# Optimization experiments

Hardware: AMD Instinct MI355X
Metric: run time of the kernel (lower is better)

Reference implementation:

```python
import jax, jax.numpy as jnp
import numpy as np

NUM_HEADS = 8
CHUNK = 64
TOP_K = 5


def setup_inputs() -> dict:
    key = jax.random.key(0)
    ks = jax.random.split(key, 5)
    D = 512
    x = jax.random.normal(ks[0], (1, 2048, D), dtype=jnp.float32)
    s = 0.02
    Wq = jax.random.normal(ks[1], (D, D), dtype=jnp.float32) * s
    Wk = jax.random.normal(ks[2], (D, D), dtype=jnp.float32) * s
    Wv = jax.random.normal(ks[3], (D, D), dtype=jnp.float32) * s
    Wo = jax.random.normal(ks[4], (D, D), dtype=jnp.float32) * s
    return {"x": x, "Wq": Wq, "Wk": Wk, "Wv": Wv, "Wo": Wo}


def reference(x, Wq, Wk, Wv, Wo):
    B, S, D = x.shape
    H = NUM_HEADS
    hd = D // H
    scale = hd ** -0.5
    C = S // CHUNK  # number of chunks

    def split_heads(t):
        return t.reshape(B, S, H, hd).transpose(0, 2, 1, 3)  # [B,H,S,hd]

    Q = split_heads(x @ Wq)
    K = split_heads(x @ Wk)
    V = split_heads(x @ Wv)

    # chunked K/V: [B,H,C,chunk,hd]
    Kc = K.reshape(B, H, C, CHUNK, hd)
    Vc = V.reshape(B, H, C, CHUNK, hd)

    # chunk descriptors: mean-pooled keys per chunk -> [B,H,C,hd]
    chunk_keys = Kc.mean(axis=3)

    # route each query to top-k chunks by scaled similarity
    sims = jnp.einsum('bhsd,bhcd->bhsc', Q, chunk_keys) * scale  # [B,H,S,C]
    _, idx = jax.lax.top_k(sims, TOP_K)  # [B,H,S,K]

    # gather selected K/V chunk blocks: [B,H,S,K,chunk,hd]
    idx_flat = idx.reshape(B, H, S * TOP_K)[:, :, :, None, None]
    Kg = jnp.take_along_axis(Kc, idx_flat, axis=2).reshape(B, H, S, TOP_K, CHUNK, hd)
    Vg = jnp.take_along_axis(Vc, idx_flat, axis=2).reshape(B, H, S, TOP_K, CHUNK, hd)

    # sparse block attention over the K*chunk gathered keys per query
    scores = jnp.einsum('bhsd,bhskcd->bhskc', Q, Kg) * scale
    attn = jax.nn.softmax(scores.reshape(B, H, S, TOP_K * CHUNK), axis=-1)
    attn = attn.reshape(B, H, S, TOP_K, CHUNK)
    out = jnp.einsum('bhskc,bhskcd->bhsd', attn, Vg)  # [B,H,S,hd]

    out = out.transpose(0, 2, 1, 3).reshape(B, S, D)
    return out @ Wo
```

## Files before the change

kernel.cpp:

```cpp
#include <hip/hip_runtime.h>
#include <hip/hip_bf16.h>
#include <math.h>

#define S_LEN 2048
#define D_DIM 512
#define H_NUM 8
#define HD    64
#define C_NUM 32
#define TOPK  5
#define SCALE 0.125f
#define QCAP  1024
#define ATILES 16

typedef __attribute__((ext_vector_type(8))) short bf16x8;
typedef __attribute__((ext_vector_type(4))) float f32x4;

__device__ __forceinline__ unsigned short f2b(float f) {
    __hip_bfloat16 h = __float2bfloat16(f);
    unsigned short u;
    __builtin_memcpy(&u, &h, 2);
    return u;
}
__device__ __forceinline__ bf16x8 pack8(float4 a, float4 b) {
    bf16x8 r;
    r[0] = (short)f2b(a.x); r[1] = (short)f2b(a.y);
    r[2] = (short)f2b(a.z); r[3] = (short)f2b(a.w);
    r[4] = (short)f2b(b.x); r[5] = (short)f2b(b.y);
    r[6] = (short)f2b(b.z); r[7] = (short)f2b(b.w);
    return r;
}
__device__ __forceinline__ float b2f(unsigned short u) {
    __hip_bfloat16 h;
    __builtin_memcpy(&h, &u, 2);
    return __bfloat162float(h);
}

#define BM 64
#define BN 64
#define BK 32

__device__ __forceinline__ void gemm_body(const float* __restrict__ A,
                                          const float* __restrict__ B,
                                          float* __restrict__ C,
                                          int M, int N, int K,
                                          int bx, int by) {
    __shared__ float As[BK][BM + 4];
    __shared__ float Bs[BK][BN];

    const int t  = threadIdx.x;
    const int tx = t & 15;
    const int ty = t >> 4;
    const int m0 = by * BM;
    const int n0 = bx * BN;

    float4 acc0 = make_float4(0.f,0.f,0.f,0.f);
    float4 acc1 = make_float4(0.f,0.f,0.f,0.f);
    float4 acc2 = make_float4(0.f,0.f,0.f,0.f);
    float4 acc3 = make_float4(0.f,0.f,0.f,0.f);

    const int ar = t >> 3;
    const int ac = (t & 7) * 4;
    const int br = t >> 4;
    const int bc = (t & 15) * 4;

    float4 a0, a1, b0, b1;
    auto LD = [&](int k0) {
        a0 = *(const float4*)&A[(size_t)(m0 + ar)      * K + k0 + ac];
        a1 = *(const float4*)&A[(size_t)(m0 + ar + 32) * K + k0 + ac];
        b0 = *(const float4*)&B[(size_t)(k0 + br)      * N + n0 + bc];
        b1 = *(const float4*)&B[(size_t)(k0 + br + 16) * N + n0 + bc];
    };

    LD(0);
    for (int k0 = 0; k0 < K; k0 += BK) {
        __syncthreads();
        As[ac+0][ar]    = a0.x; As[ac+1][ar]    = a0.y; As[ac+2][ar]    = a0.z; As[ac+3][ar]    = a0.w;
        As[ac+0][ar+32] = a1.x; As[ac+1][ar+32] = a1.y; As[ac+2][ar+32] = a1.z; As[ac+3][ar+32] = a1.w;
        *(float4*)&Bs[br][bc]      = b0;
        *(float4*)&Bs[br + 16][bc] = b1;
        __syncthreads();

        if (k0 + BK < K) LD(k0 + BK);

        #pragma unroll
        for (int kk = 0; kk < BK; ++kk) {
            float4 a = *(const float4*)&As[kk][ty * 4];
            float4 b = *(const float4*)&Bs[kk][tx * 4];
            acc0.x += a.x*b.x; acc0.y += a.x*b.y; acc0.z += a.x*b.z; acc0.w += a.x*b.w;
            acc1.x += a.y*b.x; acc1.y += a.y*b.y; acc1.z += a.y*b.z; acc1.w += a.y*b.w;
            acc2.x += a.z*b.x; acc2.y += a.z*b.y; acc2.z += a.z*b.z; acc2.w += a.z*b.w;
            acc3.x += a.w*b.x; acc3.y += a.w*b.y; acc3.z += a.w*b.z; acc3.w += a.w*b.w;
        }
    }

    *(float4*)&C[(size_t)(m0 + ty*4 + 0) * N + n0 + tx*4] = acc0;
    *(float4*)&C[(size_t)(m0 + ty*4 + 1) * N + n0 + tx*4] = acc1;
    *(float4*)&C[(size_t)(m0 + ty*4 + 2) * N + n0 + tx*4] = acc2;
    *(float4*)&C[(size_t)(m0 + ty*4 + 3) * N + n0 + tx*4] = acc3;
}

__device__ __forceinline__ void gemm_v_body(const float* __restrict__ A,
                                            const float* __restrict__ B,
                                            unsigned short* __restrict__ C,
                                            int M, int N, int K,
                                            int bx, int by) {
    __shared__ unsigned short Asv[64][72];
    __shared__ unsigned short Bsv[64][72];

    const int t  = threadIdx.x;
    const int m0 = by * 64;
    const int n0 = bx * 64;
    const int rl = t >> 2;
    const int c4 = (t & 3) * 16;

    const int lane = t & 63, w = t >> 6, lr = lane & 15, quad = lane >> 4;

    f32x4 acc[4] = {{0.f,0.f,0.f,0.f},{0.f,0.f,0.f,0.f},
                    {0.f,0.f,0.f,0.f},{0.f,0.f,0.f,0.f}};

    float4 fa[4], fb[4];
    auto LDA = [&](int k0) {
        const float* p = &A[(size_t)(m0 + rl) * K + k0 + c4];
        fa[0] = *(const float4*)&p[0];  fa[1] = *(const float4*)&p[4];
        fa[2] = *(const float4*)&p[8];  fa[3] = *(const float4*)&p[12];
    };
    auto LDB = [&](int k0) {
        const float* p = &B[(size_t)(k0 + rl) * N + n0 + c4];
        fb[0] = *(const float4*)&p[0];  fb[1] = *(const float4*)&p[4];
        fb[2] = *(const float4*)&p[8];  fb[3] = *(const float4*)&p[12];
    };

    LDA(0); LDB(0);
    for (int k0 = 0; k0 < K; k0 += 64) {
        __syncthreads();
        *(bf16x8*)&Asv[rl][c4]     = pack8(fa[0], fa[1]);
        *(bf16x8*)&Asv[rl][c4 + 8] = pack8(fa[2], fa[3]);
        #pragma unroll
        for (int f = 0; f < 4; ++f) {
            float4 v = fb[f];
            Bsv[c4 + f*4 + 0][rl] = f2b(v.x);
            Bsv[c4 + f*4 + 1][rl] = f2b(v.y);
            Bsv[c4 + f*4 + 2][rl] = f2b(v.z);
            Bsv[c4 + f*4 + 3][rl] = f2b(v.w);
        }
        __syncthreads();

        if (k0 + 64 < K) { LDA(k0 + 64); LDB(k0 + 64); }

        bf16x8 a0 = *(const bf16x8*)&Asv[w * 16 + lr][quad * 8];
        bf16x8 a1 = *(const bf16x8*)&Asv[w * 16 + lr][32 + quad * 8];
        #pragma unroll
        for (int nt = 0; nt < 4; ++nt) {
            bf16x8 b0 = *(const bf16x8*)&Bsv[nt * 16 + lr][quad * 8];
            bf16x8 b1 = *(const bf16x8*)&Bsv[nt * 16 + lr][32 + quad * 8];
            acc[nt] = __builtin_amdgcn_mfma_f32_16x16x32_bf16(a0, b0, acc[nt], 0, 0, 0);
            acc[nt] = __builtin_amdgcn_mfma_f32_16x16x32_bf16(a1, b1, acc[nt], 0, 0, 0);
        }
    }

    #pragma unroll
    for (int nt = 0; nt < 4; ++nt)
        #pragma unroll
        for (int r = 0; r < 4; ++r) {
            int m = m0 + w * 16 + quad * 4 + r;
            int n = n0 + nt * 16 + lr;
            C[(size_t)m * N + n] = f2b(acc[nt][r]);
        }
}

__global__ __launch_bounds__(256) void gemm_qkvz(const float* __restrict__ x,
                                                 const float* __restrict__ Wq,
                                                 const float* __restrict__ Wk,
                                                 const float* __restrict__ Wv,
                                                 float* __restrict__ Qb,
                                                 float* __restrict__ Kb,
                                                 unsigned short* __restrict__ Vbf,
                                                 int* __restrict__ cur) {
    if (blockIdx.z == 2) {
        if (blockIdx.x == 0 && blockIdx.y == 0) cur[threadIdx.x] = 0;
        gemm_v_body(x, Wv, Vbf, S_LEN, D_DIM, D_DIM, blockIdx.x, blockIdx.y);
    } else {
        const float* B = (blockIdx.z == 0) ? Wq : Wk;
        float*       C = (blockIdx.z == 0) ? Qb : Kb;
        gemm_body(x, B, C, S_LEN, D_DIM, D_DIM, blockIdx.x, blockIdx.y);
    }
}

__global__ __launch_bounds__(256) void chunk_keys_kernel(const float* __restrict__ K,
                                                         float* __restrict__ ck) {
    int i = blockIdx.x * 256 + threadIdx.x;
    int c = i >> 9;
    int d = i & 511;
    const float* p = K + (size_t)c * 64 * D_DIM + d;
    float sum = 0.f;
    #pragma unroll
    for (int r = 0; r < 64; ++r) sum += p[(size_t)r * D_DIM];
    ck[(size_t)c * D_DIM + d] = sum * (1.0f / 64.0f);
}

__global__ __launch_bounds__(256) void sims_topk(const float* __restrict__ Q,
                                                 const float* __restrict__ ck,
                                                 int* __restrict__ cur,
                                                 unsigned short* __restrict__ qlist) {
    __shared__ float qtile[64][68];
    __shared__ float cks[32][68];
    __shared__ float simsb[64][36];
    __shared__ int   lds_cnt[32];
    __shared__ int   lds_base[32];

    const int t  = threadIdx.x;
    const int s0 = blockIdx.x * 64;
    const int h  = blockIdx.y;

    if (t < 32) lds_cnt[t] = 0;

    {
        int r = t >> 2;
        #pragma unroll
        for (int i = 0; i < 4; ++i) {
            int cf4 = (t & 3) * 4 + i;
            *(float4*)&qtile[r][cf4 * 4] =
                *(const float4*)&Q[(size_t)(s0 + r) * D_DIM + h * HD + cf4 * 4];
        }
    }
    for (int i = t; i < C_NUM * 16; i += 256) {
        int c = i >> 4, df4 = i & 15;
        *(float4*)&cks[c][df4 * 4] =
            *(const float4*)&ck[(size_t)c * D_DIM + h * HD + df4 * 4];
    }
    __syncthreads();

    {
        const int sl = t >> 2, g = t & 3;
        float sa[8] = {0.f,0.f,0.f,0.f,0.f,0.f,0.f,0.f};
        #pragma unroll
        for (int d4 = 0; d4 < 16; ++d4) {
            float4 q4 = *(const float4*)&qtile[sl][d4 * 4];
            #pragma unroll
            for (int j = 0; j < 8; ++j) {
                float4 c4 = *(const float4*)&cks[g * 8 + j][d4 * 4];
                sa[j] += q4.x*c4.x + q4.y*c4.y + q4.z*c4.z + q4.w*c4.w;
            }
        }
        *(float4*)&simsb[sl][g*8 + 0] = make_float4(sa[0], sa[1], sa[2], sa[3]);
        *(float4*)&simsb[sl][g*8 + 4] = make_float4(sa[4], sa[5], sa[6], sa[7]);
    }
    __syncthreads();

    int csel[TOPK], lpos[TOPK];
    if (t < 64) {
        float sv[32];
        #pragma unroll
        for (int cq = 0; cq < 8; ++cq) {
            float4 v = *(const float4*)&simsb[t][cq * 4];
            sv[cq*4+0] = v.x; sv[cq*4+1] = v.y; sv[cq*4+2] = v.z; sv[cq*4+3] = v.w;
        }
        #pragma unroll
        for (int k = 0; k < TOPK; ++k) {
            float best = -INFINITY; int bi = 0;
            #pragma unroll
            for (int cc = 0; cc < 32; ++cc) {
                bool gt = sv[cc] > best;
                best = gt ? sv[cc] : best;
                bi   = gt ? cc : bi;
            }
            #pragma unroll
            for (int cc = 0; cc < 32; ++cc)
                if (cc == bi) sv[cc] = -INFINITY;
            csel[k] = bi;
            lpos[k] = atomicAdd(&lds_cnt[bi], 1);
        }
    }
    __syncthreads();

    if (t < 32) lds_base[t] = atomicAdd(&cur[h * 32 + t], lds_cnt[t]);
    __syncthreads();

    if (t < 64) {
        #pragma unroll
        for (int k = 0; k < TOPK; ++k) {
            int c = csel[k];
            int pos = lds_base[c] + lpos[k];
            if (pos < QCAP)
                qlist[(size_t)(h * 32 + c) * QCAP + pos] =
                    (unsigned short)((s0 + t) | (k << 11));
        }
    }
}

__global__ __launch_bounds__(256) void moc_attn6(const float* __restrict__ Q,
                                                 const float* __restrict__ K,
                                                 const unsigned short* __restrict__ Vbf,
                                                 const int* __restrict__ cnt,
                                                 const unsigned short* __restrict__ qlist,
                                                 float* __restrict__ lpart,
                                                 float* __restrict__ Opart) {
    __shared__ unsigned short Qs[64][72];
    __shared__ unsigned short Ks[64][72];
    __shared__ unsigned short VT[64][72];
    __shared__ unsigned short Ps[64][72];
    __shared__ unsigned short slist[64];

    const int hc = blockIdx.y;
    const int h  = hc >> 5;
    const int c  = hc & 31;
    const int g  = blockIdx.x;
    const int t  = threadIdx.x;

    const int count = min(cnt[hc], QCAP);
    const int base  = g * 64;
    if (base >= count) return;
    const int lim = min(count - base, 64);

    const float* Kb = K + ((size_t)c * 64) * D_DIM + h * HD;
    const unsigned short* Vb = Vbf + ((size_t)c * 64) * D_DIM + h * HD;
    const unsigned short* list = qlist + (size_t)hc * QCAP + base;

    {
        const int j  = t >> 2;
        const int d0 = (t & 3) * 16;

        const float* kr = Kb + (size_t)j * D_DIM + d0;
        float4 k0 = *(const float4*)&kr[0],  k1 = *(const float4*)&kr[4];
        float4 k2 = *(const float4*)&kr[8],  k3 = *(const float4*)&kr[12];
        *(bf16x8*)&Ks[j][d0]     = pack8(k0, k1);
        *(bf16x8*)&Ks[j][d0 + 8] = pack8(k2, k3);

        const unsigned short* vr = Vb + (size_t)j * D_DIM + d0;
        bf16x8 v0 = *(const bf16x8*)&vr[0];
        bf16x8 v1 = *(const bf16x8*)&vr[8];
        #pragma unroll
        for (int i = 0; i < 8; ++i) {
            VT[d0 + i][j]     = (unsigned short)v0[i];
            VT[d0 + 8 + i][j] = (unsigned short)v1[i];
        }

        unsigned short pv = (j < lim) ? list[j] : (unsigned short)0xFFFF;
        if ((t & 3) == 0) slist[j] = pv;
        int s = (pv == 0xFFFF) ? 0 : (int)(pv & 2047);
        const float* qr = Q + (size_t)s * D_DIM + h * HD + d0;
        float4 q0 = *(const float4*)&qr[0],  q1 = *(const float4*)&qr[4];
        float4 q2 = *(const float4*)&qr[8],  q3 = *(const float4*)&qr[12];
        *(bf16x8*)&Qs[j][d0]     = pack8(q0, q1);
        *(bf16x8*)&Qs[j][d0 + 8] = pack8(q2, q3);
    }
    __syncthreads();

    const int lane = t & 63;
    const int w    = t >> 6;
    const int lr   = lane & 15;
    const int quad = lane >> 4;

    bf16x8 aq0 = *(const bf16x8*)&Qs[w * 16 + lr][quad * 8];
    bf16x8 aq1 = *(const bf16x8*)&Qs[w * 16 + lr][32 + quad * 8];

    f32x4 acc[4];
    #pragma unroll
    for (int kt = 0; kt < 4; ++kt) {
        bf16x8 b0 = *(const bf16x8*)&Ks[kt * 16 + lr][quad * 8];
        bf16x8 b1 = *(const bf16x8*)&Ks[kt * 16 + lr][32 + quad * 8];
        f32x4 z = {0.f, 0.f, 0.f, 0.f};
        z = __builtin_amdgcn_mfma_f32_16x16x32_bf16(aq0, b0, z, 0, 0, 0);
        z = __builtin_amdgcn_mfma_f32_16x16x32_bf16(aq1, b1, z, 0, 0, 0);
        acc[kt] = z;
    }

    unsigned short pb[4][4];
    float dsum[4] = {0.f, 0.f, 0.f, 0.f};
    #pragma unroll
    for (int kt = 0; kt < 4; ++kt) {
        #pragma unroll
        for (int r = 0; r < 4; ++r) {
            unsigned short u = f2b(__expf(acc[kt][r] * SCALE));
            pb[kt][r] = u;
            dsum[r] += b2f(u);
        }
    }
    #pragma unroll
    for (int r = 0; r < 4; ++r) {
        float v = dsum[r];
        v += __shfl_xor(v, 1, 64);
        v += __shfl_xor(v, 2, 64);
        v += __shfl_xor(v, 4, 64);
        v += __shfl_xor(v, 8, 64);
        dsum[r] = v;
    }
    if (lr == 0) {
        #pragma unroll
        for (int r = 0; r < 4; ++r) {
            unsigned short sv = slist[w * 16 + quad * 4 + r];
            if (sv != 0xFFFF) {
                int kk = sv >> 11, s = sv & 2047;
                lpart[((size_t)kk * H_NUM + h) * S_LEN + s] = dsum[r];
            }
        }
    }

    #pragma unroll
    for (int kt = 0; kt < 4; ++kt)
        #pragma unroll
        for (int r = 0; r < 4; ++r)
            Ps[w * 16 + quad * 4 + r][kt * 16 + lr] = pb[kt][r];

    bf16x8 ap0 = *(const bf16x8*)&Ps[w * 16 + lr][quad * 8];
    bf16x8 ap1 = *(const bf16x8*)&Ps[w * 16 + lr][32 + quad * 8];

    #pragma unroll
    for (int dt = 0; dt < 4; ++dt) {
        bf16x8 b0 = *(const bf16x8*)&VT[dt * 16 + lr][quad * 8];
        bf16x8 b1 = *(const bf16x8*)&VT[dt * 16 + lr][32 + quad * 8];
        f32x4 z = {0.f, 0.f, 0.f, 0.f};
        z = __builtin_amdgcn_mfma_f32_16x16x32_bf16(ap0, b0, z, 0, 0, 0);
        z = __builtin_amdgcn_mfma_f32_16x16x32_bf16(ap1, b1, z, 0, 0, 0);
        #pragma unroll
        for (int r = 0; r < 4; ++r) {
            unsigned short sv = slist[w * 16 + quad * 4 + r];
            if (sv != 0xFFFF) {
                int kk = sv >> 11, s = sv & 2047;
                Opart[((((size_t)kk * H_NUM + h) * S_LEN + s) * HD) + dt * 16 + lr] = z[r];
            }
        }
    }
}

__global__ __launch_bounds__(256) void gemm_out_fused(const float* __restrict__ Opart,
                                                      const float* __restrict__ lpart,
                                                      const float* __restrict__ Wo,
                                                      float* __restrict__ out) {
    __shared__ unsigned short As[64][72];
    __shared__ unsigned short Bs[64][72];

    const int t  = threadIdx.x;
    const int m0 = blockIdx.y * 64;
    const int n0 = blockIdx.x * 64;
    const int rl = t >> 2;
    const int c4 = (t & 3) * 16;

    const int lane = t & 63, w = t >> 6, lr = lane & 15, quad = lane >> 4;
    const int N = D_DIM, K = D_DIM;

    f32x4 acc[4] = {{0.f,0.f,0.f,0.f},{0.f,0.f,0.f,0.f},
                    {0.f,0.f,0.f,0.f},{0.f,0.f,0.f,0.f}};

    float4 fa[4], fb[4];
    auto LDA = [&](int k0) {
        const int kcol = k0 + c4;
        const int h  = kcol >> 6;
        const int d0 = kcol & 63;
        const int m  = m0 + rl;
        fa[0] = make_float4(0.f,0.f,0.f,0.f);
        fa[1] = make_float4(0.f,0.f,0.f,0.f);
        fa[2] = make_float4(0.f,0.f,0.f,0.f);
        fa[3] = make_float4(0.f,0.f,0.f,0.f);
        float den = 0.f;
        #pragma unroll
        for (int r = 0; r < TOPK; ++r) {
            size_t slot = ((size_t)r * H_NUM + h) * S_LEN + m;
            const float* P = Opart + slot * HD + d0;
            float4 v0 = *(const float4*)&P[0],  v1 = *(const float4*)&P[4];
            float4 v2 = *(const float4*)&P[8],  v3 = *(const float4*)&P[12];
            fa[0].x += v0.x; fa[0].y += v0.y; fa[0].z += v0.z; fa[0].w += v0.w;
            fa[1].x += v1.x; fa[1].y += v1.y; fa[1].z += v1.z; fa[1].w += v1.w;
            fa[2].x += v2.x; fa[2].y += v2.y; fa[2].z += v2.z; fa[2].w += v2.w;
            fa[3].x += v3.x; fa[3].y += v3.y; fa[3].z += v3.z; fa[3].w += v3.w;
            den += lpart[slot];
        }
        float inv = 1.0f / den;
        #pragma unroll
        for (int f = 0; f < 4; ++f) {
            fa[f].x *= inv; fa[f].y *= inv; fa[f].z *= inv; fa[f].w *= inv;
        }
    };
    auto LDB = [&](int k0) {
        const float* p = &Wo[(size_t)(k0 + rl) * N + n0 + c4];
        fb[0] = *(const float4*)&p[0];  fb[1] = *(const float4*)&p[4];
        fb[2] = *(const float4*)&p[8];  fb[3] = *(const float4*)&p[12];
    };

    LDA(0); LDB(0);
    for (int k0 = 0; k0 < K; k0 += 64) {
        __syncthreads();
        *(bf16x8*)&As[rl][c4]     = pack8(fa[0], fa[1]);
        *(bf16x8*)&As[rl][c4 + 8] = pack8(fa[2], fa[3]);
        #pragma unroll
        for (int f = 0; f < 4; ++f) {
            float4 v = fb[f];
            Bs[c4 + f*4 + 0][rl] = f2b(v.x);
            Bs[c4 + f*4 + 1][rl] = f2b(v.y);
            Bs[c4 + f*4 + 2][rl] = f2b(v.z);
            Bs[c4 + f*4 + 3][rl] = f2b(v.w);
        }
        __syncthreads();

        if (k0 + 64 < K) { LDA(k0 + 64); LDB(k0 + 64); }

        bf16x8 a0 = *(const bf16x8*)&As[w * 16 + lr][quad * 8];
        bf16x8 a1 = *(const bf16x8*)&As[w * 16 + lr][32 + quad * 8];
        #pragma unroll
        for (int nt = 0; nt < 4; ++nt) {
            bf16x8 b0 = *(const bf16x8*)&Bs[nt * 16 + lr][quad * 8];
            bf16x8 b1 = *(const bf16x8*)&Bs[nt * 16 + lr][32 + quad * 8];
            acc[nt] = __builtin_amdgcn_mfma_f32_16x16x32_bf16(a0, b0, acc[nt], 0, 0, 0);
            acc[nt] = __builtin_amdgcn_mfma_f32_16x16x32_bf16(a1, b1, acc[nt], 0, 0, 0);
        }
    }

    #pragma unroll
    for (int nt = 0; nt < 4; ++nt)
        #pragma unroll
        for (int r = 0; r < 4; ++r) {
            int m = m0 + w * 16 + quad * 4 + r;
            int n = n0 + nt * 16 + lr;
            out[(size_t)m * N + n] = acc[nt][r];
        }
}

extern "C" void kernel_launch(void* const* d_in, const int* in_sizes, int n_in,
                              void* d_out, int out_size, void* d_ws, size_t ws_size,
                              hipStream_t stream) {
    const float* x  = (const float*)d_in[0];
    const float* Wq = (const float*)d_in[1];
    const float* Wk = (const float*)d_in[2];
    const float* Wv = (const float*)d_in[3];
    const float* Wo = (const float*)d_in[4];
    float* out = (float*)d_out;

    const size_t SD = (size_t)S_LEN * D_DIM;
    float* ws    = (float*)d_ws;
    float* Qb    = ws;
    float* Kb    = Qb + SD;
    unsigned short* Vbf = (unsigned short*)(Kb + SD);
    float* ck    = (float*)(Vbf + SD);
    float* lpart = ck + (size_t)C_NUM * D_DIM;
    int*   curb  = (int*)(lpart + (size_t)TOPK * H_NUM * S_LEN);
    unsigned short* qlst = (unsigned short*)(curb + 256);
    float* Opart = (float*)(qlst + (size_t)256 * QCAP);

    dim3 pgrid(D_DIM / 64, S_LEN / 64, 3);
    gemm_qkvz<<<pgrid, 256, 0, stream>>>(x, Wq, Wk, Wv, Qb, Kb, Vbf, curb);

    chunk_keys_kernel<<<(C_NUM * D_DIM) / 256, 256, 0, stream>>>(Kb, ck);

    dim3 rgrid(S_LEN / 64, H_NUM);
    sims_topk<<<rgrid, 256, 0, stream>>>(Qb, ck, curb, qlst);

    dim3 agrid(ATILES, H_NUM * C_NUM);
    moc_attn6<<<agrid, 256, 0, stream>>>(Qb, Kb, Vbf, curb, qlst, lpart, Opart);

    dim3 ogrid(D_DIM / 64, S_LEN / 64);
    gemm_out_fused<<<ogrid, 256, 0, stream>>>(Opart, lpart, Wo, out);
}
```

Baseline: 171.2 us.

## Fuse Q/K projections sharing A tile, merge chunk-mean into V GEMM, split output reduce

Q and K projections now run in one kernel that loads the x tile once and accumulates against both Wq and Wk, which halves A-tile traffic but doubles registers per thread. The chunk-key mean is folded into the V GEMM launch as an extra row of blocks, saving one launch. The top-k partial-output reduction and normalisation move out of the output GEMM into a separate kernel that writes bf16 into the reused Q buffer. This removes the redundant per-N-tile reductions in the GEMM at the cost of one more launch and an extra round trip through memory.

```diff
diff --git a/kernel.cpp b/kernel.cpp
--- a/kernel.cpp
+++ b/kernel.cpp
@@ -14,6 +14,7 @@
 
 typedef __attribute__((ext_vector_type(8))) short bf16x8;
 typedef __attribute__((ext_vector_type(4))) float f32x4;
+typedef __attribute__((ext_vector_type(4))) unsigned short us4;
 
 __device__ __forceinline__ unsigned short f2b(float f) {
     __hip_bfloat16 h = __float2bfloat16(f);
@@ -39,36 +40,38 @@
 #define BN 64
 #define BK 32
 
-__device__ __forceinline__ void gemm_body(const float* __restrict__ A,
-                                          const float* __restrict__ B,
-                                          float* __restrict__ C,
-                                          int M, int N, int K,
-                                          int bx, int by) {
+__global__ __launch_bounds__(256) void gemm_qk2(const float* __restrict__ A,
+                                                const float* __restrict__ Wq,
+                                                const float* __restrict__ Wk,
+                                                float* __restrict__ Qb,
+                                                float* __restrict__ Kb) {
     __shared__ float As[BK][BM + 4];
-    __shared__ float Bs[BK][BN];
+    __shared__ float Bq[BK][BN];
+    __shared__ float Bk[BK][BN];
 
     const int t  = threadIdx.x;
     const int tx = t & 15;
     const int ty = t >> 4;
-    const int m0 = by * BM;
-    const int n0 = bx * BN;
-
-    float4 acc0 = make_float4(0.f,0.f,0.f,0.f);
-    float4 acc1 = make_float4(0.f,0.f,0.f,0.f);
-    float4 acc2 = make_float4(0.f,0.f,0.f,0.f);
-    float4 acc3 = make_float4(0.f,0.f,0.f,0.f);
+    const int m0 = blockIdx.y * BM;
+    const int n0 = blockIdx.x * BN;
+    const int N = D_DIM, K = D_DIM;
+
+    float4 q0 = make_float4(0.f,0.f,0.f,0.f), q1 = q0, q2 = q0, q3 = q0;
+    float4 k0a = q0, k1a = q0, k2a = q0, k3a = q0;
 
     const int ar = t >> 3;
     const int ac = (t & 7) * 4;
     const int br = t >> 4;
     const int bc = (t & 15) * 4;
 
-    float4 a0, a1, b0, b1;
+    float4 a0, a1, bq0, bq1, bk0, bk1;
     auto LD = [&](int k0) {
-        a0 = *(const float4*)&A[(size_t)(m0 + ar)      * K + k0 + ac];
-        a1 = *(const float4*)&A[(size_t)(m0 + ar + 32) * K + k0 + ac];
-        b0 = *(const float4*)&B[(size_t)(k0 + br)      * N + n0 + bc];
-        b1 = *(const float4*)&B[(size_t)(k0 + br + 16) * N + n0 + bc];
+        a0  = *(const float4*)&A [(size_t)(m0 + ar)      * K + k0 + ac];
+        a1  = *(const float4*)&A [(size_t)(m0 + ar + 32) * K + k0 + ac];
+        bq0 = *(const float4*)&Wq[(size_t)(k0 + br)      * N + n0 + bc];
+        bq1 = *(const float4*)&Wq[(size_t)(k0 + br + 16) * N + n0 + bc];
+        bk0 = *(const float4*)&Wk[(size_t)(k0 + br)      * N + n0 + bc];
+        bk1 = *(const float4*)&Wk[(size_t)(k0 + br + 16) * N + n0 + bc];
     };
 
     LD(0);
@@ -76,27 +79,38 @@
         __syncthreads();
         As[ac+0][ar]    = a0.x; As[ac+1][ar]    = a0.y; As[ac+2][ar]    = a0.z; As[ac+3][ar]    = a0.w;
         As[ac+0][ar+32] = a1.x; As[ac+1][ar+32] = a1.y; As[ac+2][ar+32] = a1.z; As[ac+3][ar+32] = a1.w;
-        *(float4*)&Bs[br][bc]      = b0;
-        *(float4*)&Bs[br + 16][bc] = b1;
+        *(float4*)&Bq[br][bc]      = bq0;
+        *(float4*)&Bq[br + 16][bc] = bq1;
+        *(float4*)&Bk[br][bc]      = bk0;
+        *(float4*)&Bk[br + 16][bc] = bk1;
         __syncthreads();
 
         if (k0 + BK < K) LD(k0 + BK);
 
         #pragma unroll
         for (int kk = 0; kk < BK; ++kk) {
-            float4 a = *(const float4*)&As[kk][ty * 4];
-            float4 b = *(const float4*)&Bs[kk][tx * 4];
-            acc0.x += a.x*b.x; acc0.y += a.x*b.y; acc0.z += a.x*b.z; acc0.w += a.x*b.w;
-            acc1.x += a.y*b.x; acc1.y += a.y*b.y; acc1.z += a.y*b.z; acc1.w += a.y*b.w;
-            acc2.x += a.z*b.x; acc2.y += a.z*b.y; acc2.z += a.z*b.z; acc2.w += a.z*b.w;
-            acc3.x += a.w*b.x; acc3.y += a.w*b.y; acc3.z += a.w*b.z; acc3.w += a.w*b.w;
-        }
-    }
-
-    *(float4*)&C[(size_t)(m0 + ty*4 + 0) * N + n0 + tx*4] = acc0;
-    *(float4*)&C[(size_t)(m0 + ty*4 + 1) * N + n0 + tx*4] = acc1;
-    *(float4*)&C[(size_t)(m0 + ty*4 + 2) * N + n0 + tx*4] = acc2;
-    *(float4*)&C[(size_t)(m0 + ty*4 + 3) * N + n0 + tx*4] = acc3;
+            float4 a  = *(const float4*)&As[kk][ty * 4];
+            float4 b  = *(const float4*)&Bq[kk][tx * 4];
+            float4 bk = *(const float4*)&Bk[kk][tx * 4];
+            q0.x += a.x*b.x; q0.y += a.x*b.y; q0.z += a.x*b.z; q0.w += a.x*b.w;
+            q1.x += a.y*b.x; q1.y += a.y*b.y; q1.z += a.y*b.z; q1.w += a.y*b.w;
+            q2.x += a.z*b.x; q2.y += a.z*b.y; q2.z += a.z*b.z; q2.w += a.z*b.w;
+            q3.x += a.w*b.x; q3.y += a.w*b.y; q3.z += a.w*b.z; q3.w += a.w*b.w;
+            k0a.x += a.x*bk.x; k0a.y += a.x*bk.y; k0a.z += a.x*bk.z; k0a.w += a.x*bk.w;
+            k1a.x += a.y*bk.x; k1a.y += a.y*bk.y; k1a.z += a.y*bk.z; k1a.w += a.y*bk.w;
+            k2a.x += a.z*bk.x; k2a.y += a.z*bk.y; k2a.z += a.z*bk.z; k2a.w += a.z*bk.w;
+            k3a.x += a.w*bk.x; k3a.y += a.w*bk.y; k3a.z += a.w*bk.z; k3a.w += a.w*bk.w;
+        }
+    }
+
+    *(float4*)&Qb[(size_t)(m0 + ty*4 + 0) * N + n0 + tx*4] = q0;
+    *(float4*)&Qb[(size_t)(m0 + ty*4 + 1) * N + n0 + tx*4] = q1;
+    *(float4*)&Qb[(size_t)(m0 + ty*4 + 2) * N + n0 + tx*4] = q2;
+    *(float4*)&Qb[(size_t)(m0 + ty*4 + 3) * N + n0 + tx*4] = q3;
+    *(float4*)&Kb[(size_t)(m0 + ty*4 + 0) * N + n0 + tx*4] = k0a;
+    *(float4*)&Kb[(size_t)(m0 + ty*4 + 1) * N + n0 + tx*4] = k1a;
+    *(float4*)&Kb[(size_t)(m0 + ty*4 + 2) * N + n0 + tx*4] = k2a;
+    *(float4*)&Kb[(size_t)(m0 + ty*4 + 3) * N + n0 + tx*4] = k3a;
 }
 
 __device__ __forceinline__ void gemm_v_body(const float* __restrict__ A,
@@ -168,34 +182,27 @@
         }
 }
 
-__global__ __launch_bounds__(256) void gemm_qkvz(const float* __restrict__ x,
-                                                 const float* __restrict__ Wq,
-                                                 const float* __restrict__ Wk,
+__global__ __launch_bounds__(256) void gemm_v_ck(const float* __restrict__ x,
                                                  const float* __restrict__ Wv,
-                                                 float* __restrict__ Qb,
-                                                 float* __restrict__ Kb,
                                                  unsigned short* __restrict__ Vbf,
+                                                 const float* __restrict__ K,
+                                                 float* __restrict__ ck,
                                                  int* __restrict__ cur) {
-    if (blockIdx.z == 2) {
-        if (blockIdx.x == 0 && blockIdx.y == 0) cur[threadIdx.x] = 0;
-        gemm_v_body(x, Wv, Vbf, S_LEN, D_DIM, D_DIM, blockIdx.x, blockIdx.y);
-    } else {
-        const float* B = (blockIdx.z == 0) ? Wq : Wk;
-        float*       C = (blockIdx.z == 0) ? Qb : Kb;
-        gemm_body(x, B, C, S_LEN, D_DIM, D_DIM, blockIdx.x, blockIdx.y);
-    }
-}
-
-__global__ __launch_bounds__(256) void chunk_keys_kernel(const float* __restrict__ K,
-                                                         float* __restrict__ ck) {
-    int i = blockIdx.x * 256 + threadIdx.x;
-    int c = i >> 9;
-    int d = i & 511;
-    const float* p = K + (size_t)c * 64 * D_DIM + d;
-    float sum = 0.f;
-    #pragma unroll
-    for (int r = 0; r < 64; ++r) sum += p[(size_t)r * D_DIM];
-    ck[(size_t)c * D_DIM + d] = sum * (1.0f / 64.0f);
+    if (blockIdx.y == 32) {
+        int t = threadIdx.x;
+        if (blockIdx.x == 0) cur[t] = 0;
+        for (int i = blockIdx.x * 256 + t; i < C_NUM * D_DIM; i += 8 * 256) {
+            int c = i >> 9;
+            int d = i & 511;
+            const float* p = K + (size_t)c * 64 * D_DIM + d;
+            float sum = 0.f;
+            #pragma unroll
+            for (int r = 0; r < 64; ++r) sum += p[(size_t)r * D_DIM];
+            ck[(size_t)c * D_DIM + d] = sum * (1.0f / 64.0f);
+        }
+        return;
+    }
+    gemm_v_body(x, Wv, Vbf, S_LEN, D_DIM, D_DIM, blockIdx.x, blockIdx.y);
 }
 
 __global__ __launch_bounds__(256) void sims_topk(const float* __restrict__ Q,
@@ -423,10 +430,33 @@
     }
 }
 
-__global__ __launch_bounds__(256) void gemm_out_fused(const float* __restrict__ Opart,
-                                                      const float* __restrict__ lpart,
-                                                      const float* __restrict__ Wo,
-                                                      float* __restrict__ out) {
+__global__ __launch_bounds__(256) void reduce_norm(const float4* __restrict__ Opart4,
+                                                   const float* __restrict__ lpart,
+                                                   unsigned short* __restrict__ Obn) {
+    int i = blockIdx.x * 256 + threadIdx.x;
+    int s    = i >> 7;
+    int col4 = i & 127;
+    int h    = col4 >> 4;
+    int f4   = col4 & 15;
+    float4 acc = make_float4(0.f,0.f,0.f,0.f);
+    float  den = 0.f;
+    #pragma unroll
+    for (int k = 0; k < TOPK; ++k) {
+        size_t slot = ((size_t)k * H_NUM + h) * S_LEN + s;
+        float4 v = Opart4[slot * 16 + f4];
+        acc.x += v.x; acc.y += v.y; acc.z += v.z; acc.w += v.w;
+        den += lpart[slot];
+    }
+    float inv = 1.0f / den;
+    us4 o;
+    o[0] = f2b(acc.x * inv); o[1] = f2b(acc.y * inv);
+    o[2] = f2b(acc.z * inv); o[3] = f2b(acc.w * inv);
+    *(us4*)&Obn[(size_t)i * 4] = o;
+}
+
+__global__ __launch_bounds__(256) void gemm_out(const unsigned short* __restrict__ Obn,
+                                                const float* __restrict__ Wo,
+                                                float* __restrict__ out) {
     __shared__ unsigned short As[64][72];
     __shared__ unsigned short Bs[64][72];
 
@@ -435,41 +465,18 @@
     const int n0 = blockIdx.x * 64;
     const int rl = t >> 2;
     const int c4 = (t & 3) * 16;
+    const int N = D_DIM, K = D_DIM;
 
     const int lane = t & 63, w = t >> 6, lr = lane & 15, quad = lane >> 4;
-    const int N = D_DIM, K = D_DIM;
 
     f32x4 acc[4] = {{0.f,0.f,0.f,0.f},{0.f,0.f,0.f,0.f},
                     {0.f,0.f,0.f,0.f},{0.f,0.f,0.f,0.f}};
 
-    float4 fa[4], fb[4];
+    bf16x8 ba[2]; float4 fb[4];
     auto LDA = [&](int k0) {
-        const int kcol = k0 + c4;
-        const int h  = kcol >> 6;
-        const int d0 = kcol & 63;
-        const int m  = m0 + rl;
-        fa[0] = make_float4(0.f,0.f,0.f,0.f);
-        fa[1] = make_float4(0.f,0.f,0.f,0.f);
-        fa[2] = make_float4(0.f,0.f,0.f,0.f);
-        fa[3] = make_float4(0.f,0.f,0.f,0.f);
-        float den = 0.f;
-        #pragma unroll
-        for (int r = 0; r < TOPK; ++r) {
-            size_t slot = ((size_t)r * H_NUM + h) * S_LEN + m;
-            const float* P = Opart + slot * HD + d0;
-            float4 v0 = *(const float4*)&P[0],  v1 = *(const float4*)&P[4];
-            float4 v2 = *(const float4*)&P[8],  v3 = *(const float4*)&P[12];
-            fa[0].x += v0.x; fa[0].y += v0.y; fa[0].z += v0.z; fa[0].w += v0.w;
-            fa[1].x += v1.x; fa[1].y += v1.y; fa[1].z += v1.z; fa[1].w += v1.w;
-            fa[2].x += v2.x; fa[2].y += v2.y; fa[2].z += v2.z; fa[2].w += v2.w;
-            fa[3].x += v3.x; fa[3].y += v3.y; fa[3].z += v3.z; fa[3].w += v3.w;
-            den += lpart[slot];
-        }
-        float inv = 1.0f / den;
-        #pragma unroll
-        for (int f = 0; f < 4; ++f) {
-            fa[f].x *= inv; fa[f].y *= inv; fa[f].z *= inv; fa[f].w *= inv;
-        }
+        const unsigned short* p = &Obn[(size_t)(m0 + rl) * K + k0 + c4];
+        ba[0] = *(const bf16x8*)&p[0];
+        ba[1] = *(const bf16x8*)&p[8];
     };
     auto LDB = [&](int k0) {
         const float* p = &Wo[(size_t)(k0 + rl) * N + n0 + c4];
@@ -480,8 +487,8 @@
     LDA(0); LDB(0);
     for (int k0 = 0; k0 < K; k0 += 64) {
         __syncthreads();
-        *(bf16x8*)&As[rl][c4]     = pack8(fa[0], fa[1]);
-        *(bf16x8*)&As[rl][c4 + 8] = pack8(fa[2], fa[3]);
+        *(bf16x8*)&As[rl][c4]     = ba[0];
+        *(bf16x8*)&As[rl][c4 + 8] = ba[1];
         #pragma unroll
         for (int f = 0; f < 4; ++f) {
             float4 v = fb[f];
@@ -535,11 +542,13 @@
     int*   curb  = (int*)(lpart + (size_t)TOPK * H_NUM * S_LEN);
     unsigned short* qlst = (unsigned short*)(curb + 256);
     float* Opart = (float*)(qlst + (size_t)256 * QCAP);
-
-    dim3 pgrid(D_DIM / 64, S_LEN / 64, 3);
-    gemm_qkvz<<<pgrid, 256, 0, stream>>>(x, Wq, Wk, Wv, Qb, Kb, Vbf, curb);
-
-    chunk_keys_kernel<<<(C_NUM * D_DIM) / 256, 256, 0, stream>>>(Kb, ck);
+    unsigned short* Obn = (unsigned short*)Qb;
+
+    dim3 qkgrid(D_DIM / BN, S_LEN / BM);
+    gemm_qk2<<<qkgrid, 256, 0, stream>>>(x, Wq, Wk, Qb, Kb);
+
+    dim3 vgrid(D_DIM / 64, S_LEN / 64 + 1);
+    gemm_v_ck<<<vgrid, 256, 0, stream>>>(x, Wv, Vbf, Kb, ck, curb);
 
     dim3 rgrid(S_LEN / 64, H_NUM);
     sims_topk<<<rgrid, 256, 0, stream>>>(Qb, ck, curb, qlst);
@@ -547,6 +556,8 @@
     dim3 agrid(ATILES, H_NUM * C_NUM);
     moc_attn6<<<agrid, 256, 0, stream>>>(Qb, Kb, Vbf, curb, qlst, lpart, Opart);
 
+    reduce_norm<<<(int)(SD / 4 / 256), 256, 0, stream>>>((const float4*)Opart, lpart, Obn);
+
     dim3 ogrid(D_DIM / 64, S_LEN / 64);
-    gemm_out_fused<<<ogrid, 256, 0, stream>>>(Opart, lpart, Wo, out);
-}
+    gemm_out<<<ogrid, 256, 0, stream>>>(Obn, Wo, out);
+}
```

Measured after the change: 209.5 us. 22.3% more time.
